# Performance work log

Measured on AMD Instinct MI355X. Metric: run time of the kernel, lower is better.

The kernel has to match this reference:

```python
import jax, jax.numpy as jnp
import numpy as np

N = 100000   # nodes
E = 1600000  # edges (avg degree 16)
HID = 128    # in_feats = n_hidden
P = 100000   # pos/neg link pairs
L = 3        # GIN layers
BN_EPS = 1e-5


def setup_inputs() -> dict:
    key = jax.random.key(0)
    ks = jax.random.split(key, 16)
    s = 1.0 / np.sqrt(HID)  # ~ torch linear init scale
    inp = {
        "x": jax.random.normal(ks[0], (N, HID), jnp.float32),
        "src": jax.random.randint(ks[1], (E,), 0, N, jnp.int32),
        "dst": jax.random.randint(ks[2], (E,), 0, N, jnp.int32),
        "pos_src": jax.random.randint(ks[3], (P,), 0, N, jnp.int32),
        "pos_dst": jax.random.randint(ks[4], (P,), 0, N, jnp.int32),
        "neg_src": jax.random.randint(ks[5], (P,), 0, N, jnp.int32),
        "neg_dst": jax.random.randint(ks[6], (P,), 0, N, jnp.int32),
        "W0": jax.random.normal(ks[7], (L, HID, HID), jnp.float32) * s,
        "W1": jax.random.normal(ks[8], (L, HID, HID), jnp.float32) * s,
        "g_mlp": jnp.ones((L, HID), jnp.float32),
        "b_mlp": jnp.zeros((L, HID), jnp.float32),
        "g_apply": jnp.ones((L, HID), jnp.float32),
        "b_apply": jnp.zeros((L, HID), jnp.float32),
        "g_out": jnp.ones((L - 1, HID), jnp.float32),
        "b_out": jnp.zeros((L - 1, HID), jnp.float32),
        "pW1": jax.random.normal(ks[9], (HID, HID), jnp.float32) * s,
        "pb1": jnp.zeros((HID,), jnp.float32),
        "pW2": jax.random.normal(ks[10], (HID, HID), jnp.float32) * s,
        "pb2": jnp.zeros((HID,), jnp.float32),
        "pW3": jax.random.normal(ks[11], (1, HID), jnp.float32) * s,
        "pb3": jnp.zeros((1,), jnp.float32),
    }
    return inp


def _bn(h, g, b):
    # training-mode BatchNorm1d: batch stats, biased variance
    mu = jnp.mean(h, axis=0)
    var = jnp.mean(jnp.square(h - mu), axis=0)
    return g * (h - mu) * jax.lax.rsqrt(var + BN_EPS) + b


def reference(x, src, dst, pos_src, pos_dst, neg_src, neg_dst,
              W0, W1, g_mlp, b_mlp, g_apply, b_apply, g_out, b_out,
              pW1, pb1, pW2, pb2, pW3, pb3):
    # in-degree for mean aggregation (clamped to avoid div-by-zero)
    deg = jnp.maximum(
        jax.ops.segment_sum(jnp.ones((E,), x.dtype), dst, num_segments=N), 1.0)
    h = x
    for l in range(L):
        # GINConv, eps = 0: h_dst + mean over in-neighbors
        agg = jax.ops.segment_sum(h[src], dst, num_segments=N) / deg[:, None]
        z = h + agg
        # ApplyNodeFunc: MLP(2 layers, no bias) with inner BN+ReLU, then BN+ReLU
        m = jax.nn.relu(_bn(z @ W0[l].T, g_mlp[l], b_mlp[l]))
        m = m @ W1[l].T
        h = jax.nn.relu(_bn(m, g_apply[l], b_apply[l]))
        if l < L - 1:
            # outer BN + ReLU (dropout is identity in eval)
            h = jax.nn.relu(_bn(h, g_out[l], b_out[l]))

    def predict(hs, hd):
        t = hs * hd
        t = jax.nn.relu(t @ pW1.T + pb1)
        t = jax.nn.relu(t @ pW2.T + pb2)
        return t @ pW3.T + pb3  # [P, 1]

    h_pos = predict(h[pos_src], h[pos_dst])
    h_neg = predict(h[neg_src], h[neg_dst])
    return (h_pos, h_neg)
```

## Files before the change

kernel.cpp:

```cpp
#include <hip/hip_runtime.h>

#define HID 128
#define BN_EPS 1e-5f

typedef __bf16 bf16;
typedef __attribute__((ext_vector_type(8))) __bf16 bf16x8;
typedef __attribute__((ext_vector_type(4))) float f32x4;

__device__ __forceinline__ float bnrelu(float x, float a, float c) {
  return fmaxf(fmaf(a, x, c), 0.f);
}

__global__ void hist_k(const int* __restrict__ dst, int* __restrict__ cnt, int E) {
  int i = blockIdx.x * blockDim.x + threadIdx.x;
  if (i < E) atomicAdd(&cnt[dst[i]], 1);
}

__global__ __launch_bounds__(256)
void scan1_k(const int* __restrict__ cnt, int* __restrict__ bsum, int Nn) {
  __shared__ int red[4];
  int tid = threadIdx.x;
  int base = blockIdx.x * 1024;
  int s = 0;
#pragma unroll
  for (int u = 0; u < 4; ++u) {
    int i = base + u * 256 + tid;
    if (i < Nn) s += cnt[i];
  }
#pragma unroll
  for (int d = 1; d < 64; d <<= 1) s += __shfl_xor(s, d, 64);
  int lane = tid & 63, wv = tid >> 6;
  if (lane == 0) red[wv] = s;
  __syncthreads();
  if (tid == 0) bsum[blockIdx.x] = red[0] + red[1] + red[2] + red[3];
}

__global__ void scan2_k(int* __restrict__ bsum, int G) {
  int lane = threadIdx.x;
  int carry = 0;
  for (int base = 0; base < G; base += 64) {
    int i = base + lane;
    int v = (i < G) ? bsum[i] : 0;
    int x = v;
#pragma unroll
    for (int d = 1; d < 64; d <<= 1) { int t = __shfl_up(x, d, 64); if (lane >= d) x += t; }
    if (i < G) bsum[i] = carry + x - v;
    carry += __shfl(x, 63, 64);
  }
}

__global__ __launch_bounds__(256)
void scan3_k(const int* __restrict__ cnt, const int* __restrict__ boff,
             int* __restrict__ row_start, int* __restrict__ cursor, int Nn, int E) {
  __shared__ int wtot[4];
  int tid = threadIdx.x, lane = tid & 63, wv = tid >> 6;
  int i0 = blockIdx.x * 1024 + tid * 4;
  int t0 = 0, t1 = 0, t2 = 0, t3 = 0;
  if (i0 + 3 < Nn) {
    int4 v = *(const int4*)(cnt + i0);
    t0 = v.x; t1 = v.y; t2 = v.z; t3 = v.w;
  } else {
    if (i0     < Nn) t0 = cnt[i0];
    if (i0 + 1 < Nn) t1 = cnt[i0 + 1];
    if (i0 + 2 < Nn) t2 = cnt[i0 + 2];
    if (i0 + 3 < Nn) t3 = cnt[i0 + 3];
  }
  int tsum = t0 + t1 + t2 + t3;
  int x = tsum;
#pragma unroll
  for (int d = 1; d < 64; d <<= 1) { int t = __shfl_up(x, d, 64); if (lane >= d) x += t; }
  if (lane == 63) wtot[wv] = x;
  __syncthreads();
  int wo = 0;
  for (int k = 0; k < wv; ++k) wo += wtot[k];
  int base = boff[blockIdx.x] + wo + x - tsum;
  if (i0     < Nn) { row_start[i0] = base; cursor[i0] = base; }
  if (i0 + 1 < Nn) { int v = base + t0;           row_start[i0 + 1] = v; cursor[i0 + 1] = v; }
  if (i0 + 2 < Nn) { int v = base + t0 + t1;      row_start[i0 + 2] = v; cursor[i0 + 2] = v; }
  if (i0 + 3 < Nn) { int v = base + t0 + t1 + t2; row_start[i0 + 3] = v; cursor[i0 + 3] = v; }
  if (blockIdx.x == 0 && tid == 0) row_start[Nn] = E;
}

__global__ void fill_k(const int* __restrict__ src, const int* __restrict__ dst,
                       int* __restrict__ cursor, int* __restrict__ csr, int E) {
  int i = blockIdx.x * blockDim.x + threadIdx.x;
  if (i < E) { int p = atomicAdd(&cursor[dst[i]], 1); csr[p] = src[i]; }
}

__global__ __launch_bounds__(256)
void wconv_k(const float* __restrict__ W0, const float* __restrict__ W1,
             const float* __restrict__ pW1, const float* __restrict__ pW2,
             bf16* __restrict__ Wb) {
  int idx = (blockIdx.x * 256 + threadIdx.x) * 4;
  int seg = idx >> 14, loc = idx & 16383;
  const float* srcp = seg < 3 ? W0 + (size_t)seg * 16384
                    : seg < 6 ? W1 + (size_t)(seg - 3) * 16384
                    : seg == 6 ? pW1 : pW2;
  float4 v = *(const float4*)(srcp + loc);
  union { bf16 h[4]; unsigned long long u; } pk;
  pk.h[0] = (bf16)v.x; pk.h[1] = (bf16)v.y; pk.h[2] = (bf16)v.z; pk.h[3] = (bf16)v.w;
  *(unsigned long long*)(Wb + idx) = pk.u;
}

template<int MODE>
__global__ __launch_bounds__(256)
void agg_k(const float* __restrict__ H,
           const float* __restrict__ ac1, const float* __restrict__ g1, const float* __restrict__ b1,
           const float* __restrict__ ac2, const float* __restrict__ g2, const float* __restrict__ b2,
           float invN,
           const int* __restrict__ row_start, const int* __restrict__ csr,
           bf16* __restrict__ Z, int Nn) {
  __shared__ float sA2[128], sC2[128], sA3[128], sC3[128];
  int tid = threadIdx.x;
  if (MODE) {
    if (tid < 128) {
      float mu = ac1[tid] * invN;
      float var = fmaxf(ac1[128 + tid] * invN - mu * mu, 0.f);
      float a = g1[tid] * rsqrtf(var + BN_EPS);
      sA2[tid] = a; sC2[tid] = fmaf(-a, mu, b1[tid]);
      mu = ac2[tid] * invN;
      var = fmaxf(ac2[128 + tid] * invN - mu * mu, 0.f);
      a = g2[tid] * rsqrtf(var + BN_EPS);
      sA3[tid] = a; sC3[tid] = fmaf(-a, mu, b2[tid]);
    }
    __syncthreads();
  }
  int wv = tid >> 6, lane = tid & 63;
  int n = blockIdx.x * 4 + wv;
  if (n >= Nn) return;
  int c0 = lane * 2;
  float A2x = 0, A2y = 0, C2x = 0, C2y = 0, A3x = 0, A3y = 0, C3x = 0, C3y = 0;
  if (MODE) {
    A2x = sA2[c0]; A2y = sA2[c0 + 1]; C2x = sC2[c0]; C2y = sC2[c0 + 1];
    A3x = sA3[c0]; A3y = sA3[c0 + 1]; C3x = sC3[c0]; C3y = sC3[c0 + 1];
  }
  int beg = row_start[n], end = row_start[n + 1];
  float2 hn = *(const float2*)(H + (size_t)n * HID + c0);
  float inv = 1.f / fmaxf((float)(end - beg), 1.f);
  float ax0 = 0, ay0 = 0, ax1 = 0, ay1 = 0, ax2 = 0, ay2 = 0, ax3 = 0, ay3 = 0;
  int j = beg;
  for (; j + 4 <= end; j += 4) {
    int s0 = csr[j], s1 = csr[j + 1], s2 = csr[j + 2], s3 = csr[j + 3];
    float2 v0 = *(const float2*)(H + (size_t)s0 * HID + c0);
    float2 v1 = *(const float2*)(H + (size_t)s1 * HID + c0);
    float2 v2 = *(const float2*)(H + (size_t)s2 * HID + c0);
    float2 v3 = *(const float2*)(H + (size_t)s3 * HID + c0);
    if (MODE) {
      v0.x = bnrelu(bnrelu(v0.x, A2x, C2x), A3x, C3x);
      v0.y = bnrelu(bnrelu(v0.y, A2y, C2y), A3y, C3y);
      v1.x = bnrelu(bnrelu(v1.x, A2x, C2x), A3x, C3x);
      v1.y = bnrelu(bnrelu(v1.y, A2y, C2y), A3y, C3y);
      v2.x = bnrelu(bnrelu(v2.x, A2x, C2x), A3x, C3x);
      v2.y = bnrelu(bnrelu(v2.y, A2y, C2y), A3y, C3y);
      v3.x = bnrelu(bnrelu(v3.x, A2x, C2x), A3x, C3x);
      v3.y = bnrelu(bnrelu(v3.y, A2y, C2y), A3y, C3y);
    }
    ax0 += v0.x; ay0 += v0.y; ax1 += v1.x; ay1 += v1.y;
    ax2 += v2.x; ay2 += v2.y; ax3 += v3.x; ay3 += v3.y;
  }
  for (; j < end; ++j) {
    int s = csr[j];
    float2 v = *(const float2*)(H + (size_t)s * HID + c0);
    if (MODE) {
      v.x = bnrelu(bnrelu(v.x, A2x, C2x), A3x, C3x);
      v.y = bnrelu(bnrelu(v.y, A2y, C2y), A3y, C3y);
    }
    ax0 += v.x; ay0 += v.y;
  }
  float ax = (ax0 + ax1) + (ax2 + ax3);
  float ay = (ay0 + ay1) + (ay2 + ay3);
  float hx = hn.x, hy = hn.y;
  if (MODE) {
    hx = bnrelu(bnrelu(hx, A2x, C2x), A3x, C3x);
    hy = bnrelu(bnrelu(hy, A2y, C2y), A3y, C3y);
  }
  float zx = hx + ax * inv, zy = hy + ay * inv;
  union { bf16 h[2]; unsigned u; } pk;
  pk.h[0] = (bf16)zx; pk.h[1] = (bf16)zy;
  *(unsigned*)((char*)Z + ((size_t)n * HID + c0) * 2) = pk.u;
}

template<int AMODE>
__global__ __launch_bounds__(256)
void gemm_k(const void* __restrict__ Asrc,
            const float* __restrict__ acIn, const float* __restrict__ g, const float* __restrict__ b,
            float invN,
            const bf16* __restrict__ Wb, float* __restrict__ C,
            float* __restrict__ accumOut, int Nrows) {
  __shared__ float sA[128], sC[128], sSum[128], sSq[128];
  int tid = threadIdx.x;
  if (tid < 128) {
    sSum[tid] = 0.f; sSq[tid] = 0.f;
    if (AMODE) {
      float mu = acIn[tid] * invN;
      float var = fmaxf(acIn[128 + tid] * invN - mu * mu, 0.f);
      float a = g[tid] * rsqrtf(var + BN_EPS);
      sA[tid] = a; sC[tid] = fmaf(-a, mu, b[tid]);
    }
  }
  __syncthreads();
  int wv = tid >> 6, lane = tid & 63;
  int lm = lane & 15, lg = lane >> 4;
  int rowbase = blockIdx.x * 128 + wv * 32;
  f32x4 acc[2][8] = {};
#pragma unroll
  for (int kk = 0; kk < 4; ++kk) {
    int kb = kk * 32 + lg * 8;
    bf16x8 af[2];
    if (AMODE == 0) {
      const bf16* Zp = (const bf16*)Asrc;
#pragma unroll
      for (int rt = 0; rt < 2; ++rt) {
        int row = rowbase + rt * 16 + lm; if (row > Nrows - 1) row = Nrows - 1;
        af[rt] = *(const bf16x8*)(Zp + (size_t)row * HID + kb);
      }
    } else {
      const float* Tp = (const float*)Asrc;
      float4 a0 = *(const float4*)(sA + kb), a1 = *(const float4*)(sA + kb + 4);
      float4 q0 = *(const float4*)(sC + kb), q1 = *(const float4*)(sC + kb + 4);
#pragma unroll
      for (int rt = 0; rt < 2; ++rt) {
        int row = rowbase + rt * 16 + lm; if (row > Nrows - 1) row = Nrows - 1;
        const float* p = Tp + (size_t)row * HID + kb;
        float4 x0 = *(const float4*)p, x1 = *(const float4*)(p + 4);
        bf16x8 f;
        f[0] = (bf16)bnrelu(x0.x, a0.x, q0.x); f[1] = (bf16)bnrelu(x0.y, a0.y, q0.y);
        f[2] = (bf16)bnrelu(x0.z, a0.z, q0.z); f[3] = (bf16)bnrelu(x0.w, a0.w, q0.w);
        f[4] = (bf16)bnrelu(x1.x, a1.x, q1.x); f[5] = (bf16)bnrelu(x1.y, a1.y, q1.y);
        f[6] = (bf16)bnrelu(x1.z, a1.z, q1.z); f[7] = (bf16)bnrelu(x1.w, a1.w, q1.w);
        af[rt] = f;
      }
    }
    bf16x8 bfr[8];
#pragma unroll
    for (int ct = 0; ct < 8; ++ct)
      bfr[ct] = *(const bf16x8*)(Wb + (size_t)(ct * 16 + lm) * HID + kb);
#pragma unroll
    for (int rt = 0; rt < 2; ++rt)
#pragma unroll
      for (int ct = 0; ct < 8; ++ct)
        acc[rt][ct] = __builtin_amdgcn_mfma_f32_16x16x32_bf16(af[rt], bfr[ct], acc[rt][ct], 0, 0, 0);
  }
#pragma unroll
  for (int ct = 0; ct < 8; ++ct) {
    int col = ct * 16 + lm;
    float ps = 0.f, pq = 0.f;
#pragma unroll
    for (int rt = 0; rt < 2; ++rt) {
#pragma unroll
      for (int i = 0; i < 4; ++i) {
        int row = rowbase + rt * 16 + lg * 4 + i;
        if (row < Nrows) {
          float v = acc[rt][ct][i];
          C[(size_t)row * HID + col] = v;
          ps += v; pq = fmaf(v, v, pq);
        }
      }
    }
    ps += __shfl_xor(ps, 16, 64); ps += __shfl_xor(ps, 32, 64);
    pq += __shfl_xor(pq, 16, 64); pq += __shfl_xor(pq, 32, 64);
    if (lane < 16) { atomicAdd(&sSum[col], ps); atomicAdd(&sSq[col], pq); }
  }
  __syncthreads();
  if (tid < 128) {
    atomicAdd(&accumOut[tid], sSum[tid]);
    atomicAdd(&accumOut[128 + tid], sSq[tid]);
  }
}

__global__ __launch_bounds__(256)
void stats1_k(const float* __restrict__ T, const float* __restrict__ acIn,
              const float* __restrict__ g, const float* __restrict__ b, float invN,
              float* __restrict__ accumOut, int Nrows) {
  int col = threadIdx.x & 127, half = threadIdx.x >> 7;
  float mu = acIn[col] * invN;
  float var = fmaxf(acIn[128 + col] * invN - mu * mu, 0.f);
  float av = g[col] * rsqrtf(var + BN_EPS);
  float cv = fmaf(-av, mu, b[col]);
  float s = 0.f, sq = 0.f;
  for (int r = blockIdx.x * 2 + half; r < Nrows; r += gridDim.x * 2) {
    float x = T[(size_t)r * HID + col];
    x = fmaxf(fmaf(av, x, cv), 0.f);
    s += x; sq = fmaf(x, x, sq);
  }
  __shared__ float sb[256], qb[256];
  sb[threadIdx.x] = s; qb[threadIdx.x] = sq;
  __syncthreads();
  if (half == 0) {
    s += sb[threadIdx.x + 128]; sq += qb[threadIdx.x + 128];
    atomicAdd(&accumOut[col], s); atomicAdd(&accumOut[128 + col], sq);
  }
}

__global__ __launch_bounds__(256)
void pred_k(const float* __restrict__ T, const float* __restrict__ acIn,
            const float* __restrict__ g, const float* __restrict__ b, float invN,
            const int* __restrict__ ps, const int* __restrict__ pd,
            const int* __restrict__ ns, const int* __restrict__ nd,
            const bf16* __restrict__ W1b, const float* __restrict__ b1p,
            const bf16* __restrict__ W2b, const float* __restrict__ b2p,
            const float* __restrict__ w3, const float* __restrict__ b3,
            float* __restrict__ out, int Pn) {
  __shared__ bf16 At[128 * 128];
  __shared__ float sAp[128], sCp[128];
  int tid = threadIdx.x;
  if (tid < 128) {
    float mu = acIn[tid] * invN;
    float var = fmaxf(acIn[128 + tid] * invN - mu * mu, 0.f);
    float a = g[tid] * rsqrtf(var + BN_EPS);
    sAp[tid] = a; sCp[tid] = fmaf(-a, mu, b[tid]);
  }
  __syncthreads();
  int q0 = blockIdx.x * 128;
  {
    int r = tid >> 1;
    int q = q0 + r;
    int cb = (tid & 1) * 64;
    if (q < 2 * Pn) {
      int s, d;
      if (q < Pn) { s = ps[q]; d = pd[q]; } else { s = ns[q - Pn]; d = nd[q - Pn]; }
      const float* rs_ = T + (size_t)s * HID;
      const float* rd_ = T + (size_t)d * HID;
      for (int c = cb; c < cb + 64; c += 4) {
        float4 xs = *(const float4*)(rs_ + c);
        float4 xd = *(const float4*)(rd_ + c);
        float4 av = *(const float4*)(sAp + c);
        float4 cv = *(const float4*)(sCp + c);
        float t0 = bnrelu(xs.x, av.x, cv.x) * bnrelu(xd.x, av.x, cv.x);
        float t1 = bnrelu(xs.y, av.y, cv.y) * bnrelu(xd.y, av.y, cv.y);
        float t2 = bnrelu(xs.z, av.z, cv.z) * bnrelu(xd.z, av.z, cv.z);
        float t3 = bnrelu(xs.w, av.w, cv.w) * bnrelu(xd.w, av.w, cv.w);
        union { bf16 h[4]; unsigned long long u; } pk;
        pk.h[0] = (bf16)t0; pk.h[1] = (bf16)t1; pk.h[2] = (bf16)t2; pk.h[3] = (bf16)t3;
        unsigned addr = (unsigned)(r * 256 + c * 2);
        addr ^= (unsigned)((r & 7) << 4);
        *(unsigned long long*)((char*)At + addr) = pk.u;
      }
    } else {
      for (int c = cb; c < cb + 64; c += 4) {
        unsigned addr = (unsigned)(r * 256 + c * 2);
        addr ^= (unsigned)((r & 7) << 4);
        *(unsigned long long*)((char*)At + addr) = 0ull;
      }
    }
  }
  __syncthreads();
  int wv = tid >> 6, lane = tid & 63;
  int lm = lane & 15, lg = lane >> 4;
  const f32x4 vzero = {0.f, 0.f, 0.f, 0.f};
  f32x4 acc[2][8];
#pragma unroll
  for (int r = 0; r < 2; ++r) for (int c = 0; c < 8; ++c) acc[r][c] = vzero;
#pragma unroll
  for (int kk = 0; kk < 4; ++kk) {
    bf16x8 af[2];
#pragma unroll
    for (int rt = 0; rt < 2; ++rt) {
      int row = wv * 32 + rt * 16 + lm;
      unsigned addr = (unsigned)(row * 256 + kk * 64 + lg * 16);
      addr ^= (unsigned)((row & 7) << 4);
      af[rt] = *(const bf16x8*)((char*)At + addr);
    }
    bf16x8 bfr[8];
#pragma unroll
    for (int ct = 0; ct < 8; ++ct)
      bfr[ct] = *(const bf16x8*)(W1b + (size_t)(ct * 16 + lm) * HID + kk * 32 + lg * 8);
#pragma unroll
    for (int rt = 0; rt < 2; ++rt)
#pragma unroll
      for (int ct = 0; ct < 8; ++ct)
        acc[rt][ct] = __builtin_amdgcn_mfma_f32_16x16x32_bf16(af[rt], bfr[ct], acc[rt][ct], 0, 0, 0);
  }
  __syncthreads();
#pragma unroll
  for (int rt = 0; rt < 2; ++rt)
#pragma unroll
    for (int ct = 0; ct < 8; ++ct) {
      int col = ct * 16 + lm;
      float bb = b1p[col];
#pragma unroll
      for (int i = 0; i < 4; ++i) {
        int row = wv * 32 + rt * 16 + lg * 4 + i;
        float v = fmaxf(acc[rt][ct][i] + bb, 0.f);
        unsigned addr = (unsigned)(row * 256 + col * 2);
        addr ^= (unsigned)((row & 7) << 4);
        *(bf16*)((char*)At + addr) = (bf16)v;
      }
    }
  __syncthreads();
#pragma unroll
  for (int r = 0; r < 2; ++r) for (int c = 0; c < 8; ++c) acc[r][c] = vzero;
#pragma unroll
  for (int kk = 0; kk < 4; ++kk) {
    bf16x8 af[2];
#pragma unroll
    for (int rt = 0; rt < 2; ++rt) {
      int row = wv * 32 + rt * 16 + lm;
      unsigned addr = (unsigned)(row * 256 + kk * 64 + lg * 16);
      addr ^= (unsigned)((row & 7) << 4);
      af[rt] = *(const bf16x8*)((char*)At + addr);
    }
    bf16x8 bfr[8];
#pragma unroll
    for (int ct = 0; ct < 8; ++ct)
      bfr[ct] = *(const bf16x8*)(W2b + (size_t)(ct * 16 + lm) * HID + kk * 32 + lg * 8);
#pragma unroll
    for (int rt = 0; rt < 2; ++rt)
#pragma unroll
      for (int ct = 0; ct < 8; ++ct)
        acc[rt][ct] = __builtin_amdgcn_mfma_f32_16x16x32_bf16(af[rt], bfr[ct], acc[rt][ct], 0, 0, 0);
  }
  float b2v[8], w3v[8];
#pragma unroll
  for (int ct = 0; ct < 8; ++ct) { b2v[ct] = b2p[ct * 16 + lm]; w3v[ct] = w3[ct * 16 + lm]; }
  float b3s = b3[0];
#pragma unroll
  for (int rt = 0; rt < 2; ++rt) {
#pragma unroll
    for (int i = 0; i < 4; ++i) {
      float p = 0.f;
#pragma unroll
      for (int ct = 0; ct < 8; ++ct)
        p += fmaxf(acc[rt][ct][i] + b2v[ct], 0.f) * w3v[ct];
      p += __shfl_xor(p, 1); p += __shfl_xor(p, 2);
      p += __shfl_xor(p, 4); p += __shfl_xor(p, 8);
      int row = wv * 32 + rt * 16 + lg * 4 + i;
      int q = q0 + row;
      if (lm == 0 && q < 2 * Pn) out[q] = p + b3s;
    }
  }
}

extern "C" void kernel_launch(void* const* d_in, const int* in_sizes, int n_in,
                              void* d_out, int out_size, void* d_ws, size_t ws_size,
                              hipStream_t stream) {
  const float* x  = (const float*)d_in[0];
  const int* src  = (const int*)d_in[1];
  const int* dst  = (const int*)d_in[2];
  const int* ps   = (const int*)d_in[3];
  const int* pd   = (const int*)d_in[4];
  const int* ns   = (const int*)d_in[5];
  const int* nd   = (const int*)d_in[6];
  const float* W0 = (const float*)d_in[7];
  const float* W1 = (const float*)d_in[8];
  const float* g_mlp   = (const float*)d_in[9];
  const float* b_mlp   = (const float*)d_in[10];
  const float* g_apply = (const float*)d_in[11];
  const float* b_apply = (const float*)d_in[12];
  const float* g_out   = (const float*)d_in[13];
  const float* b_out   = (const float*)d_in[14];
  const float* pW1 = (const float*)d_in[15];
  const float* pb1 = (const float*)d_in[16];
  const float* pW2 = (const float*)d_in[17];
  const float* pb2 = (const float*)d_in[18];
  const float* pW3 = (const float*)d_in[19];
  const float* pb3 = (const float*)d_in[20];
  float* out = (float*)d_out;

  const int N = in_sizes[0] / HID;
  const int E = in_sizes[1];
  const int P = in_sizes[3];

  char* w = (char*)d_ws;
  size_t off = 0;
  auto alloc = [&](size_t bytes) -> void* {
    void* p = w + off;
    off = (off + bytes + 255) & ~(size_t)255;
    return p;
  };
  bf16*  Z  = (bf16*)alloc((size_t)N * HID * 2);
  float* TA = (float*)alloc((size_t)N * HID * 4);
  float* TB = (float*)alloc((size_t)N * HID * 4);
  int*   csr = (int*)alloc((size_t)E * 4);
  int*   row_start = (int*)alloc((size_t)(N + 1) * 4);
  size_t zoff = off;
  int*   cnt    = (int*)alloc((size_t)N * 4);
  float* accum  = (float*)alloc(9 * 256 * 4);
  size_t zbytes = off - zoff;
  int*   cursor = (int*)alloc((size_t)N * 4);
  int*   bsum   = (int*)alloc(256 * 4);
  bf16*  Wb     = (bf16*)alloc(8 * 16384 * 2);
  (void)ws_size; (void)n_in; (void)out_size;

  const int G = (N + 1023) / 1024;
  const float invN = 1.f / (float)N;

  hipMemsetAsync(w + zoff, 0, zbytes, stream);
  int gridE = (E + 255) / 256;
  hist_k<<<gridE, 256, 0, stream>>>(dst, cnt, E);
  scan1_k<<<G, 256, 0, stream>>>(cnt, bsum, N);
  scan2_k<<<1, 64, 0, stream>>>(bsum, G);
  scan3_k<<<G, 256, 0, stream>>>(cnt, bsum, row_start, cursor, N, E);
  fill_k<<<gridE, 256, 0, stream>>>(src, dst, cursor, csr, E);
  wconv_k<<<128, 256, 0, stream>>>(W0, W1, pW1, pW2, Wb);

  int gridN4 = (N + 3) / 4;
  int gridG  = (N + 127) / 128;

  for (int l = 0; l < 3; ++l) {
    int s0 = l * 3 + 0, s1 = l * 3 + 1, s2 = l * 3 + 2;
    if (l == 0)
      agg_k<0><<<gridN4, 256, 0, stream>>>(x, nullptr, nullptr, nullptr,
                                           nullptr, nullptr, nullptr, invN,
                                           row_start, csr, Z, N);
    else {
      int p1 = (l - 1) * 3 + 1, p2 = (l - 1) * 3 + 2;
      agg_k<1><<<gridN4, 256, 0, stream>>>(TB,
                                           accum + p1 * 256, g_apply + (l - 1) * HID, b_apply + (l - 1) * HID,
                                           accum + p2 * 256, g_out + (l - 1) * HID, b_out + (l - 1) * HID,
                                           invN, row_start, csr, Z, N);
    }
    gemm_k<0><<<gridG, 256, 0, stream>>>(Z, nullptr, nullptr, nullptr, invN,
                                         Wb + (size_t)l * 16384, TA, accum + s0 * 256, N);
    gemm_k<1><<<gridG, 256, 0, stream>>>(TA, accum + s0 * 256, g_mlp + l * HID, b_mlp + l * HID, invN,
                                         Wb + (size_t)(3 + l) * 16384, TB, accum + s1 * 256, N);
    if (l < 2)
      stats1_k<<<512, 256, 0, stream>>>(TB, accum + s1 * 256, g_apply + l * HID, b_apply + l * HID,
                                        invN, accum + s2 * 256, N);
  }
  int gridP = (2 * P + 127) / 128;
  pred_k<<<gridP, 256, 0, stream>>>(TB, accum + 7 * 256, g_apply + 2 * HID, b_apply + 2 * HID, invN,
                                    ps, pd, ns, nd,
                                    Wb + (size_t)6 * 16384, pb1,
                                    Wb + (size_t)7 * 16384, pb2,
                                    pW3, pb3, out, P);
}
```

Before: 1.107 ms.

## Build CSR via two-pass bucketed partition instead of global atomic scatter

Replaces the per-edge global atomic fill of the CSR with a two-level partition. Edges are first bucketed into 64 coarse destination ranges of 2048 nodes using block-local atomics and one global atomic per bucket per block. They are then placed per node with shared-memory counters, which cuts global atomic contention and makes the scatter writes more local. It also unrolls the neighbor gather loop from 4 to 8 to keep more loads in flight. The cost is an extra E-sized buffer, two extra launches, and a fill2 stage with only about 49 blocks, which may underuse the GPU.

```diff
diff --git a/kernel.cpp b/kernel.cpp
--- a/kernel.cpp
+++ b/kernel.cpp
@@ -51,7 +51,7 @@
 
 __global__ __launch_bounds__(256)
 void scan3_k(const int* __restrict__ cnt, const int* __restrict__ boff,
-             int* __restrict__ row_start, int* __restrict__ cursor, int Nn, int E) {
+             int* __restrict__ row_start, int Nn, int E) {
   __shared__ int wtot[4];
   int tid = threadIdx.x, lane = tid & 63, wv = tid >> 6;
   int i0 = blockIdx.x * 1024 + tid * 4;
@@ -74,17 +74,67 @@
   int wo = 0;
   for (int k = 0; k < wv; ++k) wo += wtot[k];
   int base = boff[blockIdx.x] + wo + x - tsum;
-  if (i0     < Nn) { row_start[i0] = base; cursor[i0] = base; }
-  if (i0 + 1 < Nn) { int v = base + t0;           row_start[i0 + 1] = v; cursor[i0 + 1] = v; }
-  if (i0 + 2 < Nn) { int v = base + t0 + t1;      row_start[i0 + 2] = v; cursor[i0 + 2] = v; }
-  if (i0 + 3 < Nn) { int v = base + t0 + t1 + t2; row_start[i0 + 3] = v; cursor[i0 + 3] = v; }
+  if (i0     < Nn) row_start[i0] = base;
+  if (i0 + 1 < Nn) row_start[i0 + 1] = base + t0;
+  if (i0 + 2 < Nn) row_start[i0 + 2] = base + t0 + t1;
+  if (i0 + 3 < Nn) row_start[i0 + 3] = base + t0 + t1 + t2;
   if (blockIdx.x == 0 && tid == 0) row_start[Nn] = E;
 }
 
-__global__ void fill_k(const int* __restrict__ src, const int* __restrict__ dst,
-                       int* __restrict__ cursor, int* __restrict__ csr, int E) {
-  int i = blockIdx.x * blockDim.x + threadIdx.x;
-  if (i < E) { int p = atomicAdd(&cursor[dst[i]], 1); csr[p] = src[i]; }
+__global__ void init64_k(const int* __restrict__ row_start, int* __restrict__ bcur64,
+                         int Nn, int NB2) {
+  int i = threadIdx.x;
+  if (i < NB2) {
+    int n = i << 11; if (n > Nn) n = Nn;
+    bcur64[i] = row_start[n];
+  }
+}
+
+__global__ __launch_bounds__(256)
+void part64_k(const int* __restrict__ src, const int* __restrict__ dst,
+              int* __restrict__ bcur64, unsigned* __restrict__ ebuf2, int E) {
+  __shared__ int lcnt[64], gbase[64], lcur[64];
+  int tid = threadIdx.x;
+  if (tid < 64) { lcnt[tid] = 0; lcur[tid] = 0; }
+  __syncthreads();
+  int base = blockIdx.x * 2048;
+  int ok[8]; unsigned pk[8]; int bk[8];
+#pragma unroll
+  for (int u = 0; u < 8; ++u) {
+    int e = base + u * 256 + tid;
+    if (e < E) {
+      int s = src[e], d = dst[e];
+      ok[u] = 1; bk[u] = d >> 11;
+      pk[u] = ((unsigned)(d & 2047) << 17) | (unsigned)s;
+      atomicAdd(&lcnt[bk[u]], 1);
+    } else ok[u] = 0;
+  }
+  __syncthreads();
+  if (tid < 64 && lcnt[tid]) gbase[tid] = atomicAdd(&bcur64[tid], lcnt[tid]);
+  __syncthreads();
+#pragma unroll
+  for (int u = 0; u < 8; ++u) if (ok[u]) {
+    int sl = atomicAdd(&lcur[bk[u]], 1);
+    ebuf2[gbase[bk[u]] + sl] = pk[u];
+  }
+}
+
+__global__ __launch_bounds__(1024)
+void fill2_k(const unsigned* __restrict__ ebuf2, const int* __restrict__ row_start,
+             int* __restrict__ csr, int Nn) {
+  __shared__ int ncur[2048];
+  int tid = threadIdx.x;
+  ncur[tid] = 0; ncur[tid + 1024] = 0;
+  __syncthreads();
+  int nb0 = blockIdx.x << 11;
+  int hi = nb0 + 2048; if (hi > Nn) hi = Nn;
+  int beg = row_start[nb0], end = row_start[hi];
+  for (int e = beg + tid; e < end; e += 1024) {
+    unsigned v = ebuf2[e];
+    int dl = v >> 17, s = (int)(v & 0x1FFFF);
+    int p = atomicAdd(&ncur[dl], 1);
+    csr[row_start[nb0 + dl] + p] = s;
+  }
 }
 
 __global__ __launch_bounds__(256)
@@ -139,24 +189,31 @@
   float inv = 1.f / fmaxf((float)(end - beg), 1.f);
   float ax0 = 0, ay0 = 0, ax1 = 0, ay1 = 0, ax2 = 0, ay2 = 0, ax3 = 0, ay3 = 0;
   int j = beg;
-  for (; j + 4 <= end; j += 4) {
+  for (; j + 8 <= end; j += 8) {
     int s0 = csr[j], s1 = csr[j + 1], s2 = csr[j + 2], s3 = csr[j + 3];
+    int s4 = csr[j + 4], s5 = csr[j + 5], s6 = csr[j + 6], s7 = csr[j + 7];
     float2 v0 = *(const float2*)(H + (size_t)s0 * HID + c0);
     float2 v1 = *(const float2*)(H + (size_t)s1 * HID + c0);
     float2 v2 = *(const float2*)(H + (size_t)s2 * HID + c0);
     float2 v3 = *(const float2*)(H + (size_t)s3 * HID + c0);
+    float2 v4 = *(const float2*)(H + (size_t)s4 * HID + c0);
+    float2 v5 = *(const float2*)(H + (size_t)s5 * HID + c0);
+    float2 v6 = *(const float2*)(H + (size_t)s6 * HID + c0);
+    float2 v7 = *(const float2*)(H + (size_t)s7 * HID + c0);
     if (MODE) {
-      v0.x = bnrelu(bnrelu(v0.x, A2x, C2x), A3x, C3x);
-      v0.y = bnrelu(bnrelu(v0.y, A2y, C2y), A3y, C3y);
-      v1.x = bnrelu(bnrelu(v1.x, A2x, C2x), A3x, C3x);
-      v1.y = bnrelu(bnrelu(v1.y, A2y, C2y), A3y, C3y);
-      v2.x = bnrelu(bnrelu(v2.x, A2x, C2x), A3x, C3x);
-      v2.y = bnrelu(bnrelu(v2.y, A2y, C2y), A3y, C3y);
-      v3.x = bnrelu(bnrelu(v3.x, A2x, C2x), A3x, C3x);
-      v3.y = bnrelu(bnrelu(v3.y, A2y, C2y), A3y, C3y);
+      v0.x = bnrelu(bnrelu(v0.x, A2x, C2x), A3x, C3x); v0.y = bnrelu(bnrelu(v0.y, A2y, C2y), A3y, C3y);
+      v1.x = bnrelu(bnrelu(v1.x, A2x, C2x), A3x, C3x); v1.y = bnrelu(bnrelu(v1.y, A2y, C2y), A3y, C3y);
+      v2.x = bnrelu(bnrelu(v2.x, A2x, C2x), A3x, C3x); v2.y = bnrelu(bnrelu(v2.y, A2y, C2y), A3y, C3y);
+      v3.x = bnrelu(bnrelu(v3.x, A2x, C2x), A3x, C3x); v3.y = bnrelu(bnrelu(v3.y, A2y, C2y), A3y, C3y);
+      v4.x = bnrelu(bnrelu(v4.x, A2x, C2x), A3x, C3x); v4.y = bnrelu(bnrelu(v4.y, A2y, C2y), A3y, C3y);
+      v5.x = bnrelu(bnrelu(v5.x, A2x, C2x), A3x, C3x); v5.y = bnrelu(bnrelu(v5.y, A2y, C2y), A3y, C3y);
+      v6.x = bnrelu(bnrelu(v6.x, A2x, C2x), A3x, C3x); v6.y = bnrelu(bnrelu(v6.y, A2y, C2y), A3y, C3y);
+      v7.x = bnrelu(bnrelu(v7.x, A2x, C2x), A3x, C3x); v7.y = bnrelu(bnrelu(v7.y, A2y, C2y), A3y, C3y);
     }
     ax0 += v0.x; ay0 += v0.y; ax1 += v1.x; ay1 += v1.y;
     ax2 += v2.x; ay2 += v2.y; ax3 += v3.x; ay3 += v3.y;
+    ax0 += v4.x; ay0 += v4.y; ax1 += v5.x; ay1 += v5.y;
+    ax2 += v6.x; ay2 += v6.y; ax3 += v7.x; ay3 += v7.y;
   }
   for (; j < end; ++j) {
     int s = csr[j];
@@ -460,6 +517,7 @@
   const int N = in_sizes[0] / HID;
   const int E = in_sizes[1];
   const int P = in_sizes[3];
+  const int NB2 = (N + 2047) >> 11;
 
   char* w = (char*)d_ws;
   size_t off = 0;
@@ -468,18 +526,19 @@
     off = (off + bytes + 255) & ~(size_t)255;
     return p;
   };
-  bf16*  Z  = (bf16*)alloc((size_t)N * HID * 2);
-  float* TA = (float*)alloc((size_t)N * HID * 4);
-  float* TB = (float*)alloc((size_t)N * HID * 4);
+  bf16*  Z   = (bf16*)alloc((size_t)N * HID * 2);
+  float* TA  = (float*)alloc((size_t)N * HID * 4);
+  float* TB  = (float*)alloc((size_t)N * HID * 4);
   int*   csr = (int*)alloc((size_t)E * 4);
+  unsigned* ebuf2 = (unsigned*)alloc((size_t)E * 4);
   int*   row_start = (int*)alloc((size_t)(N + 1) * 4);
   size_t zoff = off;
-  int*   cnt    = (int*)alloc((size_t)N * 4);
-  float* accum  = (float*)alloc(9 * 256 * 4);
+  int*   cnt   = (int*)alloc((size_t)N * 4);
+  float* accum = (float*)alloc(9 * 256 * 4);
   size_t zbytes = off - zoff;
-  int*   cursor = (int*)alloc((size_t)N * 4);
   int*   bsum   = (int*)alloc(256 * 4);
-  bf16*  Wb     = (bf16*)alloc(8 * 16384 * 2);
+  int*   bcur64 = (int*)alloc(64 * 4);
+  bf16*  Wb = (bf16*)alloc(8 * 16384 * 2);
   (void)ws_size; (void)n_in; (void)out_size;
 
   const int G = (N + 1023) / 1024;
@@ -490,8 +549,10 @@
   hist_k<<<gridE, 256, 0, stream>>>(dst, cnt, E);
   scan1_k<<<G, 256, 0, stream>>>(cnt, bsum, N);
   scan2_k<<<1, 64, 0, stream>>>(bsum, G);
-  scan3_k<<<G, 256, 0, stream>>>(cnt, bsum, row_start, cursor, N, E);
-  fill_k<<<gridE, 256, 0, stream>>>(src, dst, cursor, csr, E);
+  scan3_k<<<G, 256, 0, stream>>>(cnt, bsum, row_start, N, E);
+  init64_k<<<1, 64, 0, stream>>>(row_start, bcur64, N, NB2);
+  part64_k<<<(E + 2047) / 2048, 256, 0, stream>>>(src, dst, bcur64, ebuf2, E);
+  fill2_k<<<NB2, 1024, 0, stream>>>(ebuf2, row_start, csr, N);
   wconv_k<<<128, 256, 0, stream>>>(W0, W1, pW1, pW2, Wb);
 
   int gridN4 = (N + 3) / 4;
```

After: 1.048 ms. 1.06x faster.
